# Kernel tuning notes

Measured on AMD Instinct MI355X. Metric: run time of the kernel, lower is better.

The kernel has to match this reference:

```python
import jax, jax.numpy as jnp
import numpy as np

TOP_K = 8
CAPACITY = 512  # >> mean load (T*K/E = 256); overflow probability is negligible

def _silu(x):
    return x * jax.nn.sigmoid(x)

def setup_inputs() -> dict:
    key = jax.random.key(0)
    ks = jax.random.split(key, 7)
    B, S, H, E, I, Is = 2, 1024, 1024, 64, 512, 2048
    s = 0.05
    return {
        "hidden_states": jax.random.normal(ks[0], (B, S, H), jnp.float32),
        "gate_w": jax.random.normal(ks[1], (H, E), jnp.float32) * s,
        "shared_gate_w": jax.random.normal(ks[2], (H, 1), jnp.float32) * s,
        "shared_gate_up_w": jax.random.normal(ks[3], (H, 2 * Is), jnp.float32) * s,
        "shared_down_w": jax.random.normal(ks[4], (Is, H), jnp.float32) * s,
        "expert_gate_up_w": jax.random.normal(ks[5], (E, H, 2 * I), jnp.float32) * s,
        "expert_down_w": jax.random.normal(ks[6], (E, I, H), jnp.float32) * s,
    }

def reference(hidden_states, gate_w, shared_gate_w, shared_gate_up_w, shared_down_w, expert_gate_up_w, expert_down_w):
    B, S, H = hidden_states.shape
    x = hidden_states.reshape(-1, H)                      # [T,H]
    T = x.shape[0]
    E = gate_w.shape[1]
    Is = shared_gate_up_w.shape[1] // 2
    I = expert_gate_up_w.shape[2] // 2

    # ---- shared expert (SwiGLU) with sigmoid token gate ----
    gu = x @ shared_gate_up_w                              # [T,2Is]
    shared = (_silu(gu[:, :Is]) * gu[:, Is:]) @ shared_down_w
    shared = shared * jax.nn.sigmoid(x @ shared_gate_w)    # [T,H]

    # ---- router: fp32 softmax -> top-k -> renormalize ----
    logits = x @ gate_w                                    # [T,E]
    probs = jax.nn.softmax(logits.astype(jnp.float32), axis=-1)
    w, idx = jax.lax.top_k(probs, TOP_K)                   # [T,K]
    w = (w / jnp.sum(w, axis=-1, keepdims=True)).astype(x.dtype)

    # ---- dispatch tokens to per-expert buffers (gather/scatter) ----
    e_flat = idx.reshape(-1)                               # [A] assignments
    w_flat = w.reshape(-1)
    A = e_flat.shape[0]
    tok = jnp.arange(A) // TOP_K                           # source token per assignment
    onehot = jax.nn.one_hot(e_flat, E, dtype=jnp.int32)    # [A,E]
    pos = jnp.take_along_axis(jnp.cumsum(onehot, axis=0) - 1, e_flat[:, None], axis=1)[:, 0]
    slot = jnp.minimum(pos, CAPACITY)                      # overflow -> dummy slot
    buf = jnp.zeros((E, CAPACITY + 1, H), x.dtype).at[e_flat, slot].set(x[tok])

    # ---- grouped expert SwiGLU ----
    gu_e = jnp.einsum('ech,ehf->ecf', buf, expert_gate_up_w)   # [E,C+1,2I]
    act = _silu(gu_e[..., :I]) * gu_e[..., I:]
    out_e = jnp.einsum('eci,eih->ech', act, expert_down_w)     # [E,C+1,H]

    # ---- combine ----
    y = out_e[e_flat, slot] * w_flat[:, None]              # [A,H]
    y = jnp.where((pos < CAPACITY)[:, None], y, jnp.zeros_like(y))
    y = y.reshape(T, TOP_K, H).sum(axis=1)                 # [T,H]

    return (y + shared).reshape(B, S, H)
```

## Files before the change

### kernel.cpp

```cpp
#include <hip/hip_runtime.h>
#include <math.h>

#define T_TOK 2048
#define H_DIM 1024
#define E_NUM 64
#define KTOP 8
#define CAP  512
#define I_DIM 512
#define IS_DIM 2048

#define LDSTR 40

typedef __attribute__((ext_vector_type(8))) _Float16 half8;
typedef __attribute__((ext_vector_type(4))) _Float16 half4v;
typedef __attribute__((ext_vector_type(4))) float f32x4;

__device__ __forceinline__ float sigm(float x){ return 1.f/(1.f+__expf(-x)); }

__global__ __launch_bounds__(256)
void k_tcvt(const float* __restrict__ S, _Float16* __restrict__ D, int K, int N)
{
  __shared__ float T[64][65];
  const size_t so = (size_t)blockIdx.z*K*N;
  const int n0 = blockIdx.x*64, k0 = blockIdx.y*64;
  const int tid = threadIdx.x;
  #pragma unroll
  for (int i=0;i<4;++i){
    int id = tid + i*256;
    int r = id >> 4, c = (id & 15)*4;
    float4 v = *(const float4*)(S + so + (size_t)(k0+r)*N + n0 + c);
    T[r][c]=v.x; T[r][c+1]=v.y; T[r][c+2]=v.z; T[r][c+3]=v.w;
  }
  __syncthreads();
  #pragma unroll
  for (int i=0;i<2;++i){
    int id = tid + i*256;
    int n = id >> 3, kc = (id & 7)*8;
    half8 h;
    #pragma unroll
    for (int j=0;j<8;++j) h[j] = (_Float16)T[kc+j][n];
    *(half8*)(D + so + (size_t)(n0+n)*K + k0 + kc) = h;
  }
}

__global__ __launch_bounds__(256)
void k_cvtx(const float* __restrict__ X, _Float16* __restrict__ Xh)
{
  size_t i = ((size_t)blockIdx.x*256 + threadIdx.x)*4;
  float4 v = *(const float4*)(X + i);
  half4v h = { (_Float16)v.x, (_Float16)v.y, (_Float16)v.z, (_Float16)v.w };
  *(half4v*)(Xh + i) = h;
}

__global__ __launch_bounds__(256)
void k_logits(const float* __restrict__ X, const float* __restrict__ GW,
              const float* __restrict__ SGW, float* __restrict__ logits,
              float* __restrict__ gate_tok)
{
  __shared__ float Xs[32*33];
  __shared__ float Ws[32*64];
  __shared__ float SGWs[32];
  __shared__ float red[256];
  const int tid = threadIdx.x;
  const int t0 = blockIdx.x * 32;
  const int tx = tid & 15, ty = tid >> 4;
  const int tg = tid & 31, qq = tid >> 5;
  float acc[2][4] = {};
  float gacc = 0.f;

  for (int k0 = 0; k0 < H_DIM; k0 += 32) {
    {
      int row = tid >> 3, c4 = (tid & 7)*4;
      float4 v = *(const float4*)(X + (size_t)(t0+row)*H_DIM + k0 + c4);
      Xs[row*33+c4+0]=v.x; Xs[row*33+c4+1]=v.y; Xs[row*33+c4+2]=v.z; Xs[row*33+c4+3]=v.w;
    }
    #pragma unroll
    for (int i=0;i<2;++i){
      int id = tid + i*256;
      int kk = id >> 4, c4 = (id & 15)*4;
      *(float4*)(Ws + kk*64 + c4) = *(const float4*)(GW + (size_t)(k0+kk)*E_NUM + c4);
    }
    if (tid < 32) SGWs[tid] = SGW[k0 + tid];
    __syncthreads();
    #pragma unroll 8
    for (int k=0;k<32;++k){
      float b[4];
      #pragma unroll
      for(int j=0;j<4;++j) b[j] = Ws[k*64 + tx*4 + j];
      #pragma unroll
      for(int i=0;i<2;++i){
        float a = Xs[(ty*2+i)*33 + k];
        #pragma unroll
        for(int j=0;j<4;++j) acc[i][j] = fmaf(a, b[j], acc[i][j]);
      }
    }
    #pragma unroll
    for (int k=0;k<4;++k)
      gacc = fmaf(Xs[tg*33 + qq*4 + k], SGWs[qq*4+k], gacc);
    __syncthreads();
  }
  #pragma unroll
  for(int i=0;i<2;++i){
    float4 o = {acc[i][0],acc[i][1],acc[i][2],acc[i][3]};
    *(float4*)(logits + (size_t)(t0+ty*2+i)*E_NUM + tx*4) = o;
  }
  red[tid] = gacc; __syncthreads();
  if (tid < 32) {
    float g = 0.f;
    #pragma unroll
    for (int p=0;p<8;++p) g += red[tid + p*32];
    gate_tok[t0+tid] = sigm(g);
  }
}

__global__ __launch_bounds__(256)
void k_topk(const float* __restrict__ logits,
            int* __restrict__ counts, int* __restrict__ etok, float* __restrict__ ew)
{
  const int tid = threadIdx.x;
  const int lane = tid & 63, w = tid >> 6;
  const int t = blockIdx.x*4 + w;
  float curv = logits[(size_t)t*E_NUM + lane];
  int curi = lane;
  float topv[KTOP]; int topi[KTOP];
  #pragma unroll
  for (int r = 0; r < KTOP; ++r) {
    float bv = curv; int bi = curi;
    #pragma unroll
    for (int off = 32; off > 0; off >>= 1) {
      float ov = __shfl_xor(bv, off);
      int oi = __shfl_xor(bi, off);
      if (ov > bv || (ov == bv && oi < bi)) { bv = ov; bi = oi; }
    }
    topv[r] = bv; topi[r] = bi;
    if (curi == bi) curv = -INFINITY;
  }
  if (lane == 0) {
    float m = topv[0], s = 0.f, wv[KTOP];
    #pragma unroll
    for (int r = 0; r < KTOP; ++r){ wv[r] = __expf(topv[r]-m); s += wv[r]; }
    float inv = 1.f/s;
    for (int r = 0; r < KTOP; ++r) {
      int ee = topi[r];
      int pos = atomicAdd(&counts[ee], 1);
      if (pos < CAP) {
        etok[ee*CAP + pos] = t;
        ew[ee*CAP + pos] = wv[r]*inv;
      }
    }
  }
}


__device__ __forceinline__ void loadA2(const _Float16* __restrict__ base, int ldk, int k0,
                                       int tid, half8 r[2]) {
  #pragma unroll
  for (int i=0;i<2;++i){
    int id = tid + i*256;
    int m = id >> 2, kc = (id & 3)*8;
    r[i] = *(const half8*)(base + (size_t)m*ldk + k0 + kc);
  }
}
__device__ __forceinline__ void storeA(_Float16* As, int tid, const half8 r[2]) {
  #pragma unroll
  for (int i=0;i<2;++i){
    int id = tid + i*256;
    int m = id >> 2, kc = (id & 3)*8;
    *(half8*)(As + m*LDSTR + kc) = r[i];
  }
}
__device__ __forceinline__ void loadB2(const _Float16* __restrict__ Bt, int ldk,
                                       int r0, int r1, int k0, int tid, half8 r[2]) {
  #pragma unroll
  for (int i=0;i<2;++i){
    int id = tid + i*256;
    int n = id >> 2, kc = (id & 3)*8;
    int grow = (n < 64) ? (r0 + n) : (r1 + n - 64);
    r[i] = *(const half8*)(Bt + (size_t)grow*ldk + k0 + kc);
  }
}
__device__ __forceinline__ void storeB(_Float16* Bs, int tid, const half8 r[2]) {
  #pragma unroll
  for (int i=0;i<2;++i){
    int id = tid + i*256;
    int n = id >> 2, c = id & 3;
    *(half8*)(Bs + n*LDSTR + ((c ^ ((n>>3)&3))*8)) = r[i];
  }
}

__device__ __forceinline__ void mfma_tiles_h(const _Float16* As, const _Float16* Bs,
                                             int wy, const int* bidx, int lane, f32x4 acc[4][4])
{
  const int lm = lane & 15, q = lane >> 4;
  half8 a[4];
  #pragma unroll
  for (int mt = 0; mt < 4; ++mt)
    a[mt] = *(const half8*)(As + (wy*64 + mt*16 + lm)*LDSTR + q*8);
  #pragma unroll
  for (int nt = 0; nt < 4; ++nt) {
    int n = bidx[nt]*16 + lm;
    half8 b = *(const half8*)(Bs + n*LDSTR + ((q ^ ((n>>3)&3))*8));
    #pragma unroll
    for (int mt = 0; mt < 4; ++mt)
      acc[mt][nt] = __builtin_amdgcn_mfma_f32_16x16x32_f16(a[mt], b, acc[mt][nt], 0,0,0);
  }
}

#define DECL_LDS \
  __shared__ __align__(16) _Float16 As[128*LDSTR]; \
  __shared__ __align__(16) _Float16 Bs[128*LDSTR];

#define ZERO_ACC \
  f32x4 acc[4][4]; \
  _Pragma("unroll") for (int a_=0;a_<4;++a_) _Pragma("unroll") for (int b_=0;b_<4;++b_) \
    acc[a_][b_] = (f32x4){0.f,0.f,0.f,0.f};

__global__ __launch_bounds__(256,3)
void k_gu_shared(const _Float16* __restrict__ Xh, const _Float16* __restrict__ Wt,
                 _Float16* __restrict__ O)
{
  DECL_LDS
  const int tid = threadIdx.x, lane = tid & 63, wave = tid >> 6;
  const int wx = wave & 1, wy = wave >> 1;
  const int m0 = blockIdx.y * 128;
  const int gn0 = blockIdx.x * 64;
  ZERO_ACC
  const int bidx[4] = {2*wx, 2*wx+1, 4+2*wx, 5+2*wx};
  const _Float16* Ab = Xh + (size_t)m0*H_DIM;

  half8 ra[2], rb[2];
  loadA2(Ab, H_DIM, 0, tid, ra);
  loadB2(Wt, H_DIM, gn0, IS_DIM + gn0, 0, tid, rb);
  for (int k0 = 0; k0 < H_DIM; k0 += 32) {
    storeA(As, tid, ra); storeB(Bs, tid, rb);
    __syncthreads();
    if (k0 + 32 < H_DIM) {
      loadA2(Ab, H_DIM, k0+32, tid, ra);
      loadB2(Wt, H_DIM, gn0, IS_DIM + gn0, k0+32, tid, rb);
    }
    mfma_tiles_h(As, Bs, wy, bidx, lane, acc);
    __syncthreads();
  }
  const int lm = lane & 15, q = lane >> 4;
  #pragma unroll
  for (int mt = 0; mt < 4; ++mt) {
    int m = m0 + wy*64 + mt*16 + q*4;
    #pragma unroll
    for (int jj = 0; jj < 2; ++jj) {
      int col = gn0 + (2*wx + jj)*16 + lm;
      #pragma unroll
      for (int r = 0; r < 4; ++r) {
        float g = acc[mt][jj][r], u = acc[mt][2+jj][r];
        O[(size_t)(m + r)*IS_DIM + col] = (_Float16)(g * sigm(g) * u);
      }
    }
  }
}

__global__ __launch_bounds__(256,3)
void k_dn_shared(const _Float16* __restrict__ S, const _Float16* __restrict__ Wt,
                 const float* __restrict__ gate_tok, float* __restrict__ OUT)
{
  DECL_LDS
  const int tid = threadIdx.x, lane = tid & 63, wave = tid >> 6;
  const int wx = wave & 1, wy = wave >> 1;
  const int m0 = blockIdx.y * 128;
  const int n0 = blockIdx.x * 128;
  ZERO_ACC
  const int bidx[4] = {4*wx, 4*wx+1, 4*wx+2, 4*wx+3};
  const _Float16* Ab = S + (size_t)m0*IS_DIM;

  half8 ra[2], rb[2];
  loadA2(Ab, IS_DIM, 0, tid, ra);
  loadB2(Wt, IS_DIM, n0, n0 + 64, 0, tid, rb);
  for (int k0 = 0; k0 < IS_DIM; k0 += 32) {
    storeA(As, tid, ra); storeB(Bs, tid, rb);
    __syncthreads();
    if (k0 + 32 < IS_DIM) {
      loadA2(Ab, IS_DIM, k0+32, tid, ra);
      loadB2(Wt, IS_DIM, n0, n0 + 64, k0+32, tid, rb);
    }
    mfma_tiles_h(As, Bs, wy, bidx, lane, acc);
    __syncthreads();
  }
  const int lm = lane & 15, q = lane >> 4;
  #pragma unroll
  for (int mt = 0; mt < 4; ++mt) {
    int m = m0 + wy*64 + mt*16 + q*4;
    #pragma unroll
    for (int r = 0; r < 4; ++r) {
      float gt = gate_tok[m + r];
      #pragma unroll
      for (int nt = 0; nt < 4; ++nt) {
        int col = n0 + wx*64 + nt*16 + lm;
        OUT[(size_t)(m + r)*H_DIM + col] = acc[mt][nt][r] * gt;
      }
    }
  }
}

__global__ __launch_bounds__(256,3)
void k_gu_expert(const _Float16* __restrict__ Xh, const _Float16* __restrict__ Wt,
                 const int* __restrict__ counts, const int* __restrict__ etok,
                 _Float16* __restrict__ O, int e_base)
{
  const int el = blockIdx.z, e = e_base + el;
  int cnt = counts[e]; if (cnt > CAP) cnt = CAP;
  const int m0 = blockIdx.y * 128;
  if (m0 >= cnt) return;
  const int gn0 = blockIdx.x * 64;
  DECL_LDS
  const int tid = threadIdx.x, lane = tid & 63, wave = tid >> 6;
  const int wx = wave & 1, wy = wave >> 1;
  ZERO_ACC
  const int bidx[4] = {2*wx, 2*wx+1, 4+2*wx, 5+2*wx};
  const _Float16* Wb = Wt + (size_t)e*H_DIM*(2*I_DIM);

  int t2[2];
  #pragma unroll
  for (int i = 0; i < 2; ++i) {
    int m = m0 + ((tid + i*256) >> 2);
    t2[i] = (m < cnt) ? etok[e*CAP + m] : -1;
  }

  half8 ra[2], rb[2];
  #pragma unroll
  for (int i=0;i<2;++i){
    int kc = ((tid + i*256) & 3)*8;
    ra[i] = (t2[i] >= 0) ? *(const half8*)(Xh + (size_t)t2[i]*H_DIM + kc)
                         : (half8){0,0,0,0,0,0,0,0};
  }
  loadB2(Wb, H_DIM, gn0, I_DIM + gn0, 0, tid, rb);
  for (int k0 = 0; k0 < H_DIM; k0 += 32) {
    storeA(As, tid, ra); storeB(Bs, tid, rb);
    __syncthreads();
    if (k0 + 32 < H_DIM) {
      #pragma unroll
      for (int i=0;i<2;++i){
        int kc = ((tid + i*256) & 3)*8;
        ra[i] = (t2[i] >= 0) ? *(const half8*)(Xh + (size_t)t2[i]*H_DIM + k0 + 32 + kc)
                             : (half8){0,0,0,0,0,0,0,0};
      }
      loadB2(Wb, H_DIM, gn0, I_DIM + gn0, k0+32, tid, rb);
    }
    mfma_tiles_h(As, Bs, wy, bidx, lane, acc);
    __syncthreads();
  }
  const int lm = lane & 15, q = lane >> 4;
  #pragma unroll
  for (int mt = 0; mt < 4; ++mt) {
    int m = m0 + wy*64 + mt*16 + q*4;
    #pragma unroll
    for (int jj = 0; jj < 2; ++jj) {
      int col = gn0 + (2*wx + jj)*16 + lm;
      #pragma unroll
      for (int r = 0; r < 4; ++r) {
        if (m + r < cnt) {
          float g = acc[mt][jj][r], u = acc[mt][2+jj][r];
          O[((size_t)el*CAP + m + r)*I_DIM + col] = (_Float16)(g * sigm(g) * u);
        }
      }
    }
  }
}

__global__ __launch_bounds__(256,3)
void k_dn_expert(const _Float16* __restrict__ G, const _Float16* __restrict__ Wt,
                 const int* __restrict__ counts, const int* __restrict__ etok,
                 const float* __restrict__ ew, float* __restrict__ OUT, int e_base)
{
  const int el = blockIdx.z, e = e_base + el;
  int cnt = counts[e]; if (cnt > CAP) cnt = CAP;
  const int m0 = blockIdx.y * 128;
  if (m0 >= cnt) return;
  const int n0 = blockIdx.x * 128;
  DECL_LDS
  const int tid = threadIdx.x, lane = tid & 63, wave = tid >> 6;
  const int wx = wave & 1, wy = wave >> 1;
  ZERO_ACC
  const int bidx[4] = {4*wx, 4*wx+1, 4*wx+2, 4*wx+3};
  const _Float16* Wb = Wt + (size_t)e*I_DIM*H_DIM;
  const _Float16* Ab = G + ((size_t)el*CAP + m0)*I_DIM;

  bool ok2[2];
  #pragma unroll
  for (int i=0;i<2;++i) ok2[i] = (m0 + ((tid + i*256) >> 2)) < cnt;

  half8 ra[2], rb[2];
  #pragma unroll
  for (int i=0;i<2;++i){
    int id = tid + i*256;
    int m = id >> 2, kc = (id & 3)*8;
    ra[i] = ok2[i] ? *(const half8*)(Ab + (size_t)m*I_DIM + kc) : (half8){0,0,0,0,0,0,0,0};
  }
  loadB2(Wb, I_DIM, n0, n0 + 64, 0, tid, rb);
  for (int k0 = 0; k0 < I_DIM; k0 += 32) {
    storeA(As, tid, ra); storeB(Bs, tid, rb);
    __syncthreads();
    if (k0 + 32 < I_DIM) {
      #pragma unroll
      for (int i=0;i<2;++i){
        int id = tid + i*256;
        int m = id >> 2, kc = (id & 3)*8;
        ra[i] = ok2[i] ? *(const half8*)(Ab + (size_t)m*I_DIM + k0 + 32 + kc) : (half8){0,0,0,0,0,0,0,0};
      }
      loadB2(Wb, I_DIM, n0, n0 + 64, k0+32, tid, rb);
    }
    mfma_tiles_h(As, Bs, wy, bidx, lane, acc);
    __syncthreads();
  }
  const int lm = lane & 15, q = lane >> 4;
  #pragma unroll
  for (int mt = 0; mt < 4; ++mt) {
    int m = m0 + wy*64 + mt*16 + q*4;
    #pragma unroll
    for (int r = 0; r < 4; ++r) {
      if (m + r < cnt) {
        float w = ew[e*CAP + m + r];
        int tok = etok[e*CAP + m + r];
        float* op = OUT + (size_t)tok*H_DIM;
        #pragma unroll
        for (int nt = 0; nt < 4; ++nt) {
          int col = n0 + wx*64 + nt*16 + lm;
          atomicAdd(op + col, acc[mt][nt][r] * w);
        }
      }
    }
  }
}

extern "C" void kernel_launch(void* const* d_in, const int* in_sizes, int n_in,
                              void* d_out, int out_size, void* d_ws, size_t ws_size,
                              hipStream_t stream) {
  const float* x    = (const float*)d_in[0];
  const float* gw   = (const float*)d_in[1];
  const float* sgw  = (const float*)d_in[2];
  const float* sguw = (const float*)d_in[3];
  const float* sdw  = (const float*)d_in[4];
  const float* eguw = (const float*)d_in[5];
  const float* edw  = (const float*)d_in[6];
  float* out = (float*)d_out;

  char* ws = (char*)d_ws;
  int*   counts   = (int*)(ws + 0);
  int*   etok     = (int*)(ws + 4096);
  float* ew       = (float*)(ws + 4096 + 131072);
  float* gate_tok = (float*)(ws + 4096 + 2*131072);
  float* logits   = (float*)(ws + (512u<<10));
  _Float16* plane  = (_Float16*)(ws + (1u<<20));
  _Float16* Xh     = (_Float16*)(ws + (16u<<20));
  _Float16* sguwT  = (_Float16*)(ws + (24u<<20));
  _Float16* sdwT   = (_Float16*)(ws + (32u<<20));
  _Float16* eguwT  = (_Float16*)(ws + (40u<<20));
  _Float16* edwT   = (_Float16*)(ws + (168u<<20));

  hipMemsetAsync(counts, 0, E_NUM*sizeof(int), stream);
  k_cvtx<<<T_TOK*H_DIM/1024, 256, 0, stream>>>(x, Xh);
  k_tcvt<<<dim3(4096/64, 1024/64, 1),  256, 0, stream>>>(sguw, sguwT, 1024, 4096);
  k_tcvt<<<dim3(1024/64, 2048/64, 1),  256, 0, stream>>>(sdw,  sdwT,  2048, 1024);
  k_tcvt<<<dim3(1024/64, 1024/64, 64), 256, 0, stream>>>(eguw, eguwT, 1024, 1024);
  k_tcvt<<<dim3(1024/64,  512/64, 64), 256, 0, stream>>>(edw,  edwT,   512, 1024);
  k_logits<<<T_TOK/32, 256, 0, stream>>>(x, gw, sgw, logits, gate_tok);
  k_topk<<<T_TOK/4, 256, 0, stream>>>(logits, counts, etok, ew);
  k_gu_shared<<<dim3(IS_DIM/64, T_TOK/128), 256, 0, stream>>>(Xh, sguwT, plane);
  k_dn_shared<<<dim3(H_DIM/128, T_TOK/128), 256, 0, stream>>>(plane, sdwT, gate_tok, out);
  for (int g = 0; g < 4; ++g) {
    k_gu_expert<<<dim3(I_DIM/64, CAP/128, 16), 256, 0, stream>>>(Xh, eguwT, counts, etok, plane, g*16);
    k_dn_expert<<<dim3(H_DIM/128, CAP/128, 16), 256, 0, stream>>>(plane, edwT, counts, etok, ew, out, g*16);
  }
}
```

Baseline: 966.1 us.

## Fuse router, use direct-to-LDS double-buffered GEMMs, replace atomics with combine kernel

Merges the logits and top-k kernels into one router kernel that also records per-assignment slots and weights. All GEMMs now stage tiles with global_load_lds into double-buffered LDS with BK=64 and XOR swizzling, replacing the register-staged single buffer. The per-group expert launches become a single launch over all 64 experts. The expert down projection now writes per-slot outputs to a buffer and a separate combine kernel sums them per token, replacing float atomics. This trades more LDS per block (lower occupancy) and an extra fp32 intermediate buffer for fewer launches, less atomic contention and better load overlap.

```diff
diff --git a/kernel.cpp b/kernel.cpp
--- a/kernel.cpp
+++ b/kernel.cpp
@@ -8,14 +8,19 @@
 #define CAP  512
 #define I_DIM 512
 #define IS_DIM 2048
-
-#define LDSTR 40
+#define BK 64
 
 typedef __attribute__((ext_vector_type(8))) _Float16 half8;
 typedef __attribute__((ext_vector_type(4))) _Float16 half4v;
 typedef __attribute__((ext_vector_type(4))) float f32x4;
 
 __device__ __forceinline__ float sigm(float x){ return 1.f/(1.f+__expf(-x)); }
+
+__device__ __forceinline__ void gl16(const _Float16* g, _Float16* l) {
+  __builtin_amdgcn_global_load_lds((const __attribute__((address_space(1))) void*)g,
+                                   (__attribute__((address_space(3))) void*)l,
+                                   16, 0, 0);
+}
 
 __global__ __launch_bounds__(256)
 void k_tcvt(const float* __restrict__ S, _Float16* __restrict__ D, int K, int N)
@@ -53,79 +58,47 @@
 }
 
 __global__ __launch_bounds__(256)
-void k_logits(const float* __restrict__ X, const float* __restrict__ GW,
-              const float* __restrict__ SGW, float* __restrict__ logits,
-              float* __restrict__ gate_tok)
-{
-  __shared__ float Xs[32*33];
-  __shared__ float Ws[32*64];
-  __shared__ float SGWs[32];
-  __shared__ float red[256];
-  const int tid = threadIdx.x;
-  const int t0 = blockIdx.x * 32;
-  const int tx = tid & 15, ty = tid >> 4;
-  const int tg = tid & 31, qq = tid >> 5;
-  float acc[2][4] = {};
-  float gacc = 0.f;
-
-  for (int k0 = 0; k0 < H_DIM; k0 += 32) {
-    {
-      int row = tid >> 3, c4 = (tid & 7)*4;
-      float4 v = *(const float4*)(X + (size_t)(t0+row)*H_DIM + k0 + c4);
-      Xs[row*33+c4+0]=v.x; Xs[row*33+c4+1]=v.y; Xs[row*33+c4+2]=v.z; Xs[row*33+c4+3]=v.w;
-    }
-    #pragma unroll
-    for (int i=0;i<2;++i){
-      int id = tid + i*256;
-      int kk = id >> 4, c4 = (id & 15)*4;
-      *(float4*)(Ws + kk*64 + c4) = *(const float4*)(GW + (size_t)(k0+kk)*E_NUM + c4);
-    }
-    if (tid < 32) SGWs[tid] = SGW[k0 + tid];
-    __syncthreads();
-    #pragma unroll 8
-    for (int k=0;k<32;++k){
-      float b[4];
-      #pragma unroll
-      for(int j=0;j<4;++j) b[j] = Ws[k*64 + tx*4 + j];
-      #pragma unroll
-      for(int i=0;i<2;++i){
-        float a = Xs[(ty*2+i)*33 + k];
-        #pragma unroll
-        for(int j=0;j<4;++j) acc[i][j] = fmaf(a, b[j], acc[i][j]);
-      }
-    }
-    #pragma unroll
-    for (int k=0;k<4;++k)
-      gacc = fmaf(Xs[tg*33 + qq*4 + k], SGWs[qq*4+k], gacc);
-    __syncthreads();
-  }
-  #pragma unroll
-  for(int i=0;i<2;++i){
-    float4 o = {acc[i][0],acc[i][1],acc[i][2],acc[i][3]};
-    *(float4*)(logits + (size_t)(t0+ty*2+i)*E_NUM + tx*4) = o;
-  }
-  red[tid] = gacc; __syncthreads();
-  if (tid < 32) {
-    float g = 0.f;
-    #pragma unroll
-    for (int p=0;p<8;++p) g += red[tid + p*32];
-    gate_tok[t0+tid] = sigm(g);
-  }
-}
-
-__global__ __launch_bounds__(256)
-void k_topk(const float* __restrict__ logits,
-            int* __restrict__ counts, int* __restrict__ etok, float* __restrict__ ew)
-{
-  const int tid = threadIdx.x;
-  const int lane = tid & 63, w = tid >> 6;
-  const int t = blockIdx.x*4 + w;
-  float curv = logits[(size_t)t*E_NUM + lane];
-  int curi = lane;
+void k_router(const float* __restrict__ X, const float* __restrict__ GW,
+              const float* __restrict__ SGW, int* __restrict__ counts,
+              int* __restrict__ etok, float* __restrict__ gate_tok,
+              int* __restrict__ asg, float* __restrict__ aw)
+{
+  __shared__ float Xs[4][1024];
+  __shared__ float part[4][4][64];
+  const int tid = threadIdx.x, w = tid>>6, lane = tid&63;
+  const int t0 = blockIdx.x*4;
+  #pragma unroll
+  for (int i=0;i<4;++i){
+    int idx = tid + i*256;
+    *(float4*)(&Xs[0][0] + idx*4) = *(const float4*)(X + (size_t)t0*H_DIM + idx*4);
+  }
+  __syncthreads();
+  {
+    float a0=0.f,a1=0.f,a2=0.f,a3=0.f;
+    const int kb = w*256;
+    #pragma unroll 4
+    for (int k=0;k<256;++k){
+      float gv = GW[(size_t)(kb+k)*E_NUM + lane];
+      a0 = fmaf(Xs[0][kb+k], gv, a0);
+      a1 = fmaf(Xs[1][kb+k], gv, a1);
+      a2 = fmaf(Xs[2][kb+k], gv, a2);
+      a3 = fmaf(Xs[3][kb+k], gv, a3);
+    }
+    part[w][0][lane]=a0; part[w][1][lane]=a1; part[w][2][lane]=a2; part[w][3][lane]=a3;
+  }
+  float g = 0.f;
+  #pragma unroll
+  for (int i=0;i<16;++i) g = fmaf(Xs[w][lane+64*i], SGW[lane+64*i], g);
+  #pragma unroll
+  for (int off=32;off;off>>=1) g += __shfl_xor(g, off);
+  __syncthreads();
+  const int t = t0 + w;
+  if (lane==0) gate_tok[t] = sigm(g);
+  float curv = part[0][w][lane]+part[1][w][lane]+part[2][w][lane]+part[3][w][lane];
   float topv[KTOP]; int topi[KTOP];
   #pragma unroll
   for (int r = 0; r < KTOP; ++r) {
-    float bv = curv; int bi = curi;
+    float bv = curv; int bi = lane;
     #pragma unroll
     for (int off = 32; off > 0; off >>= 1) {
       float ov = __shfl_xor(bv, off);
@@ -133,7 +106,7 @@
       if (ov > bv || (ov == bv && oi < bi)) { bv = ov; bi = oi; }
     }
     topv[r] = bv; topi[r] = bi;
-    if (curi == bi) curv = -INFINITY;
+    if (lane == bi) curv = -INFINITY;
   }
   if (lane == 0) {
     float m = topv[0], s = 0.f, wv[KTOP];
@@ -143,103 +116,107 @@
     for (int r = 0; r < KTOP; ++r) {
       int ee = topi[r];
       int pos = atomicAdd(&counts[ee], 1);
-      if (pos < CAP) {
-        etok[ee*CAP + pos] = t;
-        ew[ee*CAP + pos] = wv[r]*inv;
-      }
-    }
-  }
-}
-
-
-__device__ __forceinline__ void loadA2(const _Float16* __restrict__ base, int ldk, int k0,
-                                       int tid, half8 r[2]) {
-  #pragma unroll
-  for (int i=0;i<2;++i){
-    int id = tid + i*256;
-    int m = id >> 2, kc = (id & 3)*8;
-    r[i] = *(const half8*)(base + (size_t)m*ldk + k0 + kc);
-  }
-}
-__device__ __forceinline__ void storeA(_Float16* As, int tid, const half8 r[2]) {
-  #pragma unroll
-  for (int i=0;i<2;++i){
-    int id = tid + i*256;
-    int m = id >> 2, kc = (id & 3)*8;
-    *(half8*)(As + m*LDSTR + kc) = r[i];
-  }
-}
-__device__ __forceinline__ void loadB2(const _Float16* __restrict__ Bt, int ldk,
-                                       int r0, int r1, int k0, int tid, half8 r[2]) {
-  #pragma unroll
-  for (int i=0;i<2;++i){
-    int id = tid + i*256;
-    int n = id >> 2, kc = (id & 3)*8;
-    int grow = (n < 64) ? (r0 + n) : (r1 + n - 64);
-    r[i] = *(const half8*)(Bt + (size_t)grow*ldk + k0 + kc);
-  }
-}
-__device__ __forceinline__ void storeB(_Float16* Bs, int tid, const half8 r[2]) {
-  #pragma unroll
-  for (int i=0;i<2;++i){
-    int id = tid + i*256;
-    int n = id >> 2, c = id & 3;
-    *(half8*)(Bs + n*LDSTR + ((c ^ ((n>>3)&3))*8)) = r[i];
-  }
-}
-
-__device__ __forceinline__ void mfma_tiles_h(const _Float16* As, const _Float16* Bs,
-                                             int wy, const int* bidx, int lane, f32x4 acc[4][4])
-{
-  const int lm = lane & 15, q = lane >> 4;
-  half8 a[4];
-  #pragma unroll
-  for (int mt = 0; mt < 4; ++mt)
-    a[mt] = *(const half8*)(As + (wy*64 + mt*16 + lm)*LDSTR + q*8);
-  #pragma unroll
-  for (int nt = 0; nt < 4; ++nt) {
-    int n = bidx[nt]*16 + lm;
-    half8 b = *(const half8*)(Bs + n*LDSTR + ((q ^ ((n>>3)&3))*8));
-    #pragma unroll
-    for (int mt = 0; mt < 4; ++mt)
-      acc[mt][nt] = __builtin_amdgcn_mfma_f32_16x16x32_f16(a[mt], b, acc[mt][nt], 0,0,0);
-  }
-}
-
-#define DECL_LDS \
-  __shared__ __align__(16) _Float16 As[128*LDSTR]; \
-  __shared__ __align__(16) _Float16 Bs[128*LDSTR];
-
-#define ZERO_ACC \
-  f32x4 acc[4][4]; \
-  _Pragma("unroll") for (int a_=0;a_<4;++a_) _Pragma("unroll") for (int b_=0;b_<4;++b_) \
-    acc[a_][b_] = (f32x4){0.f,0.f,0.f,0.f};
-
-__global__ __launch_bounds__(256,3)
+      bool ok = (pos < CAP);
+      if (ok) etok[ee*CAP + pos] = t;
+      asg[t*KTOP + r] = ok ? (ee*CAP + pos) : -1;
+      aw[t*KTOP + r]  = wv[r]*inv;
+    }
+  }
+}
+
+
+template<int MT>
+__device__ __forceinline__ void stageA_lin(const _Float16* __restrict__ Ab, int ldk, int k0,
+                                           int tid, _Float16* Asb)
+{
+  const int w = tid>>6, l = tid&63, sub = l>>3, gc = (l&7) ^ sub;
+  #pragma unroll
+  for (int j=0;j<MT;++j){
+    int r = (w*MT + j)*8 + sub;
+    gl16(Ab + (size_t)r*ldk + k0 + gc*8, Asb + (w*MT+j)*512 + l*8);
+  }
+}
+__device__ __forceinline__ void stageA_ptr(const _Float16* const* bj, int k0,
+                                           int tid, _Float16* Asb)
+{
+  const int w = tid>>6, l = tid&63, gc = (l&7) ^ (l>>3);
+  #pragma unroll
+  for (int j=0;j<4;++j)
+    gl16(bj[j] + k0 + gc*8, Asb + (w*4+j)*512 + l*8);
+}
+__device__ __forceinline__ void stageB(const _Float16* __restrict__ Bt, int ldk,
+                                       int r0, int r1, int k0, int tid, _Float16* Bsb)
+{
+  const int w = tid>>6, l = tid&63, sub = l>>3, gc = (l&7) ^ sub;
+  #pragma unroll
+  for (int j=0;j<4;++j){
+    int r = (w*4+j)*8 + sub;
+    int grow = (r < 64) ? (r0 + r) : (r1 + r - 64);
+    gl16(Bt + (size_t)grow*ldk + k0 + gc*8, Bsb + (w*4+j)*512 + l*8);
+  }
+}
+
+template<int MT>
+__device__ __forceinline__ void mfma_bk64(const _Float16* As, const _Float16* Bs,
+                                          int wy, const int* bidx, int lane,
+                                          f32x4 acc[][4])
+{
+  const int lm = lane & 15, q = lane >> 4, h = lm & 7;
+  half8 a[2][MT], b[2][4];
+  #pragma unroll
+  for (int kk=0;kk<2;++kk){
+    #pragma unroll
+    for (int mt=0;mt<MT;++mt){
+      int r = wy*(MT*16) + mt*16 + lm;
+      int ch = ((kk<<2)|q) ^ h;
+      a[kk][mt] = *(const half8*)(As + r*BK + ch*8);
+    }
+    #pragma unroll
+    for (int nt=0;nt<4;++nt){
+      int n = bidx[nt]*16 + lm;
+      int ch = ((kk<<2)|q) ^ h;
+      b[kk][nt] = *(const half8*)(Bs + n*BK + ch*8);
+    }
+  }
+  #pragma unroll
+  for (int kk=0;kk<2;++kk)
+    #pragma unroll
+    for (int nt=0;nt<4;++nt)
+      #pragma unroll
+      for (int mt=0;mt<MT;++mt)
+        acc[mt][nt] = __builtin_amdgcn_mfma_f32_16x16x32_f16(a[kk][mt], b[kk][nt], acc[mt][nt], 0,0,0);
+}
+
+#define ZACC(MT_) \
+  f32x4 acc[MT_][4]; \
+  _Pragma("unroll") for (int a_=0;a_<MT_;++a_) \
+  _Pragma("unroll") for (int b_=0;b_<4;++b_) acc[a_][b_] = (f32x4){0.f,0.f,0.f,0.f};
+
+__global__ __launch_bounds__(256,2)
 void k_gu_shared(const _Float16* __restrict__ Xh, const _Float16* __restrict__ Wt,
                  _Float16* __restrict__ O)
 {
-  DECL_LDS
+  __shared__ __align__(16) _Float16 As[2][128*BK];
+  __shared__ __align__(16) _Float16 Bs[2][128*BK];
   const int tid = threadIdx.x, lane = tid & 63, wave = tid >> 6;
   const int wx = wave & 1, wy = wave >> 1;
-  const int m0 = blockIdx.y * 128;
-  const int gn0 = blockIdx.x * 64;
-  ZERO_ACC
+  const int m0 = blockIdx.y * 128, gn0 = blockIdx.x * 64;
+  ZACC(4)
   const int bidx[4] = {2*wx, 2*wx+1, 4+2*wx, 5+2*wx};
   const _Float16* Ab = Xh + (size_t)m0*H_DIM;
 
-  half8 ra[2], rb[2];
-  loadA2(Ab, H_DIM, 0, tid, ra);
-  loadB2(Wt, H_DIM, gn0, IS_DIM + gn0, 0, tid, rb);
-  for (int k0 = 0; k0 < H_DIM; k0 += 32) {
-    storeA(As, tid, ra); storeB(Bs, tid, rb);
+  stageA_lin<4>(Ab, H_DIM, 0, tid, As[0]);
+  stageB(Wt, H_DIM, gn0, IS_DIM+gn0, 0, tid, Bs[0]);
+  __syncthreads();
+  int cur = 0;
+  for (int k0 = 0; k0 < H_DIM; k0 += BK) {
+    if (k0 + BK < H_DIM) {
+      stageA_lin<4>(Ab, H_DIM, k0+BK, tid, As[cur^1]);
+      stageB(Wt, H_DIM, gn0, IS_DIM+gn0, k0+BK, tid, Bs[cur^1]);
+    }
+    mfma_bk64<4>(As[cur], Bs[cur], wy, bidx, lane, acc);
     __syncthreads();
-    if (k0 + 32 < H_DIM) {
-      loadA2(Ab, H_DIM, k0+32, tid, ra);
-      loadB2(Wt, H_DIM, gn0, IS_DIM + gn0, k0+32, tid, rb);
-    }
-    mfma_tiles_h(As, Bs, wy, bidx, lane, acc);
-    __syncthreads();
+    cur ^= 1;
   }
   const int lm = lane & 15, q = lane >> 4;
   #pragma unroll
@@ -261,32 +238,32 @@
 void k_dn_shared(const _Float16* __restrict__ S, const _Float16* __restrict__ Wt,
                  const float* __restrict__ gate_tok, float* __restrict__ OUT)
 {
-  DECL_LDS
+  __shared__ __align__(16) _Float16 As[2][64*BK];
+  __shared__ __align__(16) _Float16 Bs[2][128*BK];
   const int tid = threadIdx.x, lane = tid & 63, wave = tid >> 6;
   const int wx = wave & 1, wy = wave >> 1;
-  const int m0 = blockIdx.y * 128;
-  const int n0 = blockIdx.x * 128;
-  ZERO_ACC
+  const int m0 = blockIdx.y * 64, n0 = blockIdx.x * 128;
+  ZACC(2)
   const int bidx[4] = {4*wx, 4*wx+1, 4*wx+2, 4*wx+3};
   const _Float16* Ab = S + (size_t)m0*IS_DIM;
 
-  half8 ra[2], rb[2];
-  loadA2(Ab, IS_DIM, 0, tid, ra);
-  loadB2(Wt, IS_DIM, n0, n0 + 64, 0, tid, rb);
-  for (int k0 = 0; k0 < IS_DIM; k0 += 32) {
-    storeA(As, tid, ra); storeB(Bs, tid, rb);
+  stageA_lin<2>(Ab, IS_DIM, 0, tid, As[0]);
+  stageB(Wt, IS_DIM, n0, n0+64, 0, tid, Bs[0]);
+  __syncthreads();
+  int cur = 0;
+  for (int k0 = 0; k0 < IS_DIM; k0 += BK) {
+    if (k0 + BK < IS_DIM) {
+      stageA_lin<2>(Ab, IS_DIM, k0+BK, tid, As[cur^1]);
+      stageB(Wt, IS_DIM, n0, n0+64, k0+BK, tid, Bs[cur^1]);
+    }
+    mfma_bk64<2>(As[cur], Bs[cur], wy, bidx, lane, acc);
     __syncthreads();
-    if (k0 + 32 < IS_DIM) {
-      loadA2(Ab, IS_DIM, k0+32, tid, ra);
-      loadB2(Wt, IS_DIM, n0, n0 + 64, k0+32, tid, rb);
-    }
-    mfma_tiles_h(As, Bs, wy, bidx, lane, acc);
-    __syncthreads();
+    cur ^= 1;
   }
   const int lm = lane & 15, q = lane >> 4;
   #pragma unroll
-  for (int mt = 0; mt < 4; ++mt) {
-    int m = m0 + wy*64 + mt*16 + q*4;
+  for (int mt = 0; mt < 2; ++mt) {
+    int m = m0 + wy*32 + mt*16 + q*4;
     #pragma unroll
     for (int r = 0; r < 4; ++r) {
       float gt = gate_tok[m + r];
@@ -299,52 +276,46 @@
   }
 }
 
-__global__ __launch_bounds__(256,3)
+__global__ __launch_bounds__(256,2)
 void k_gu_expert(const _Float16* __restrict__ Xh, const _Float16* __restrict__ Wt,
                  const int* __restrict__ counts, const int* __restrict__ etok,
-                 _Float16* __restrict__ O, int e_base)
-{
-  const int el = blockIdx.z, e = e_base + el;
+                 const _Float16* __restrict__ zp, _Float16* __restrict__ O)
+{
+  const int e = blockIdx.z;
   int cnt = counts[e]; if (cnt > CAP) cnt = CAP;
   const int m0 = blockIdx.y * 128;
   if (m0 >= cnt) return;
-  const int gn0 = blockIdx.x * 64;
-  DECL_LDS
+  __shared__ __align__(16) _Float16 As[2][128*BK];
+  __shared__ __align__(16) _Float16 Bs[2][128*BK];
   const int tid = threadIdx.x, lane = tid & 63, wave = tid >> 6;
   const int wx = wave & 1, wy = wave >> 1;
-  ZERO_ACC
+  const int gn0 = blockIdx.x * 64;
+  ZACC(4)
   const int bidx[4] = {2*wx, 2*wx+1, 4+2*wx, 5+2*wx};
   const _Float16* Wb = Wt + (size_t)e*H_DIM*(2*I_DIM);
 
-  int t2[2];
-  #pragma unroll
-  for (int i = 0; i < 2; ++i) {
-    int m = m0 + ((tid + i*256) >> 2);
-    t2[i] = (m < cnt) ? etok[e*CAP + m] : -1;
-  }
-
-  half8 ra[2], rb[2];
-  #pragma unroll
-  for (int i=0;i<2;++i){
-    int kc = ((tid + i*256) & 3)*8;
-    ra[i] = (t2[i] >= 0) ? *(const half8*)(Xh + (size_t)t2[i]*H_DIM + kc)
-                         : (half8){0,0,0,0,0,0,0,0};
-  }
-  loadB2(Wb, H_DIM, gn0, I_DIM + gn0, 0, tid, rb);
-  for (int k0 = 0; k0 < H_DIM; k0 += 32) {
-    storeA(As, tid, ra); storeB(Bs, tid, rb);
+  const _Float16* bj[4];
+  {
+    const int w = tid>>6, l = tid&63, sub = l>>3;
+    #pragma unroll
+    for (int j=0;j<4;++j){
+      int m = m0 + (w*4+j)*8 + sub;
+      int t = (m < cnt) ? etok[e*CAP + m] : -1;
+      bj[j] = (t >= 0) ? (Xh + (size_t)t*H_DIM) : zp;
+    }
+  }
+  stageA_ptr(bj, 0, tid, As[0]);
+  stageB(Wb, H_DIM, gn0, I_DIM+gn0, 0, tid, Bs[0]);
+  __syncthreads();
+  int cur = 0;
+  for (int k0 = 0; k0 < H_DIM; k0 += BK) {
+    if (k0 + BK < H_DIM) {
+      stageA_ptr(bj, k0+BK, tid, As[cur^1]);
+      stageB(Wb, H_DIM, gn0, I_DIM+gn0, k0+BK, tid, Bs[cur^1]);
+    }
+    mfma_bk64<4>(As[cur], Bs[cur], wy, bidx, lane, acc);
     __syncthreads();
-    if (k0 + 32 < H_DIM) {
-      #pragma unroll
-      for (int i=0;i<2;++i){
-        int kc = ((tid + i*256) & 3)*8;
-        ra[i] = (t2[i] >= 0) ? *(const half8*)(Xh + (size_t)t2[i]*H_DIM + k0 + 32 + kc)
-                             : (half8){0,0,0,0,0,0,0,0};
-      }
-      loadB2(Wb, H_DIM, gn0, I_DIM + gn0, k0+32, tid, rb);
-    }
-    mfma_tiles_h(As, Bs, wy, bidx, lane, acc);
-    __syncthreads();
+    cur ^= 1;
   }
   const int lm = lane & 15, q = lane >> 4;
   #pragma unroll
@@ -357,57 +328,52 @@
       for (int r = 0; r < 4; ++r) {
         if (m + r < cnt) {
           float g = acc[mt][jj][r], u = acc[mt][2+jj][r];
-          O[((size_t)el*CAP + m + r)*I_DIM + col] = (_Float16)(g * sigm(g) * u);
+          O[((size_t)e*CAP + m + r)*I_DIM + col] = (_Float16)(g * sigm(g) * u);
         }
       }
     }
   }
 }
 
-__global__ __launch_bounds__(256,3)
+__global__ __launch_bounds__(256,2)
 void k_dn_expert(const _Float16* __restrict__ G, const _Float16* __restrict__ Wt,
-                 const int* __restrict__ counts, const int* __restrict__ etok,
-                 const float* __restrict__ ew, float* __restrict__ OUT, int e_base)
-{
-  const int el = blockIdx.z, e = e_base + el;
+                 const int* __restrict__ counts, const _Float16* __restrict__ zp,
+                 float* __restrict__ Oe)
+{
+  const int e = blockIdx.z;
   int cnt = counts[e]; if (cnt > CAP) cnt = CAP;
   const int m0 = blockIdx.y * 128;
   if (m0 >= cnt) return;
   const int n0 = blockIdx.x * 128;
-  DECL_LDS
+  __shared__ __align__(16) _Float16 As[2][128*BK];
+  __shared__ __align__(16) _Float16 Bs[2][128*BK];
   const int tid = threadIdx.x, lane = tid & 63, wave = tid >> 6;
   const int wx = wave & 1, wy = wave >> 1;
-  ZERO_ACC
+  ZACC(4)
   const int bidx[4] = {4*wx, 4*wx+1, 4*wx+2, 4*wx+3};
   const _Float16* Wb = Wt + (size_t)e*I_DIM*H_DIM;
-  const _Float16* Ab = G + ((size_t)el*CAP + m0)*I_DIM;
-
-  bool ok2[2];
-  #pragma unroll
-  for (int i=0;i<2;++i) ok2[i] = (m0 + ((tid + i*256) >> 2)) < cnt;
-
-  half8 ra[2], rb[2];
-  #pragma unroll
-  for (int i=0;i<2;++i){
-    int id = tid + i*256;
-    int m = id >> 2, kc = (id & 3)*8;
-    ra[i] = ok2[i] ? *(const half8*)(Ab + (size_t)m*I_DIM + kc) : (half8){0,0,0,0,0,0,0,0};
-  }
-  loadB2(Wb, I_DIM, n0, n0 + 64, 0, tid, rb);
-  for (int k0 = 0; k0 < I_DIM; k0 += 32) {
-    storeA(As, tid, ra); storeB(Bs, tid, rb);
+
+  const _Float16* bj[4];
+  {
+    const int w = tid>>6, l = tid&63, sub = l>>3;
+    #pragma unroll
+    for (int j=0;j<4;++j){
+      int m = m0 + (w*4+j)*8 + sub;
+      bj[j] = (m < cnt) ? (G + (size_t)(e*CAP + m)*I_DIM) : zp;
+    }
+  }
+  stageA_ptr(bj, 0, tid, As[0]);
+  stageB(Wb, I_DIM, n0, n0+64, 0, tid, Bs[0]);
+  __syncthreads();
+  int cur = 0;
+  for (int k0 = 0; k0 < I_DIM; k0 += BK) {
+    if (k0 + BK < I_DIM) {
+      stageA_ptr(bj, k0+BK, tid, As[cur^1]);
+      stageB(Wb, I_DIM, n0, n0+64, k0+BK, tid, Bs[cur^1]);
+    }
+    mfma_bk64<4>(As[cur], Bs[cur], wy, bidx, lane, acc);
     __syncthreads();
-    if (k0 + 32 < I_DIM) {
-      #pragma unroll
-      for (int i=0;i<2;++i){
-        int id = tid + i*256;
-        int m = id >> 2, kc = (id & 3)*8;
-        ra[i] = ok2[i] ? *(const half8*)(Ab + (size_t)m*I_DIM + k0 + 32 + kc) : (half8){0,0,0,0,0,0,0,0};
-      }
-      loadB2(Wb, I_DIM, n0, n0 + 64, k0+32, tid, rb);
-    }
-    mfma_tiles_h(As, Bs, wy, bidx, lane, acc);
-    __syncthreads();
+    cur ^= 1;
   }
   const int lm = lane & 15, q = lane >> 4;
   #pragma unroll
@@ -416,17 +382,36 @@
     #pragma unroll
     for (int r = 0; r < 4; ++r) {
       if (m + r < cnt) {
-        float w = ew[e*CAP + m + r];
-        int tok = etok[e*CAP + m + r];
-        float* op = OUT + (size_t)tok*H_DIM;
         #pragma unroll
         for (int nt = 0; nt < 4; ++nt) {
           int col = n0 + wx*64 + nt*16 + lm;
-          atomicAdd(op + col, acc[mt][nt][r] * w);
+          Oe[(size_t)(e*CAP + m + r)*H_DIM + col] = acc[mt][nt][r];
         }
       }
     }
   }
+}
+
+__global__ __launch_bounds__(256)
+void k_combine(const float* __restrict__ Oe, const int* __restrict__ asg,
+               const float* __restrict__ aw, float* __restrict__ OUT)
+{
+  __shared__ int sa[KTOP]; __shared__ float sw[KTOP];
+  const int t = blockIdx.x, tid = threadIdx.x;
+  if (tid < KTOP){ sa[tid] = asg[t*KTOP + tid]; sw[tid] = aw[t*KTOP + tid]; }
+  __syncthreads();
+  float4 acc = *(const float4*)(OUT + (size_t)t*H_DIM + tid*4);
+  #pragma unroll
+  for (int r = 0; r < KTOP; ++r) {
+    int a = sa[r];
+    if (a >= 0) {
+      float wv = sw[r];
+      float4 v = *(const float4*)(Oe + (size_t)a*H_DIM + tid*4);
+      acc.x = fmaf(v.x, wv, acc.x); acc.y = fmaf(v.y, wv, acc.y);
+      acc.z = fmaf(v.z, wv, acc.z); acc.w = fmaf(v.w, wv, acc.w);
+    }
+  }
+  *(float4*)(OUT + (size_t)t*H_DIM + tid*4) = acc;
 }
 
 extern "C" void kernel_launch(void* const* d_in, const int* in_sizes, int n_in,
@@ -442,30 +427,31 @@
   float* out = (float*)d_out;
 
   char* ws = (char*)d_ws;
-  int*   counts   = (int*)(ws + 0);
-  int*   etok     = (int*)(ws + 4096);
-  float* ew       = (float*)(ws + 4096 + 131072);
-  float* gate_tok = (float*)(ws + 4096 + 2*131072);
-  float* logits   = (float*)(ws + (512u<<10));
-  _Float16* plane  = (_Float16*)(ws + (1u<<20));
-  _Float16* Xh     = (_Float16*)(ws + (16u<<20));
-  _Float16* sguwT  = (_Float16*)(ws + (24u<<20));
-  _Float16* sdwT   = (_Float16*)(ws + (32u<<20));
-  _Float16* eguwT  = (_Float16*)(ws + (40u<<20));
-  _Float16* edwT   = (_Float16*)(ws + (168u<<20));
-
-  hipMemsetAsync(counts, 0, E_NUM*sizeof(int), stream);
+  int*      counts   = (int*)(ws + 0);
+  _Float16* zp       = (_Float16*)(ws + 4096);
+  int*      etok     = (int*)(ws + 32768);
+  int*      asg      = (int*)(ws + 163840);
+  float*    aw       = (float*)(ws + 229376);
+  float*    gate_tok = (float*)(ws + 294912);
+  _Float16* Xh       = (_Float16*)(ws + (1u<<20));
+  _Float16* plane    = (_Float16*)(ws + (8u<<20));
+  _Float16* actg     = (_Float16*)(ws + (16u<<20));
+  float*    Oe       = (float*)(ws + (48u<<20));
+  _Float16* sguwT    = (_Float16*)(ws + (176u<<20));
+  _Float16* sdwT     = (_Float16*)(ws + (184u<<20));
+  _Float16* eguwT    = (_Float16*)(ws + (192u<<20));
+  _Float16* edwT     = (_Float16*)(ws + (320u<<20));
+
+  hipMemsetAsync(ws, 0, 32768, stream);
   k_cvtx<<<T_TOK*H_DIM/1024, 256, 0, stream>>>(x, Xh);
+  k_router<<<T_TOK/4, 256, 0, stream>>>(x, gw, sgw, counts, etok, gate_tok, asg, aw);
   k_tcvt<<<dim3(4096/64, 1024/64, 1),  256, 0, stream>>>(sguw, sguwT, 1024, 4096);
   k_tcvt<<<dim3(1024/64, 2048/64, 1),  256, 0, stream>>>(sdw,  sdwT,  2048, 1024);
   k_tcvt<<<dim3(1024/64, 1024/64, 64), 256, 0, stream>>>(eguw, eguwT, 1024, 1024);
   k_tcvt<<<dim3(1024/64,  512/64, 64), 256, 0, stream>>>(edw,  edwT,   512, 1024);
-  k_logits<<<T_TOK/32, 256, 0, stream>>>(x, gw, sgw, logits, gate_tok);
-  k_topk<<<T_TOK/4, 256, 0, stream>>>(logits, counts, etok, ew);
   k_gu_shared<<<dim3(IS_DIM/64, T_TOK/128), 256, 0, stream>>>(Xh, sguwT, plane);
-  k_dn_shared<<<dim3(H_DIM/128, T_TOK/128), 256, 0, stream>>>(plane, sdwT, gate_tok, out);
-  for (int g = 0; g < 4; ++g) {
-    k_gu_expert<<<dim3(I_DIM/64, CAP/128, 16), 256, 0, stream>>>(Xh, eguwT, counts, etok, plane, g*16);
-    k_dn_expert<<<dim3(H_DIM/128, CAP/128, 16), 256, 0, stream>>>(plane, edwT, counts, etok, ew, out, g*16);
-  }
-}
+  k_dn_shared<<<dim3(H_DIM/128, T_TOK/64), 256, 0, stream>>>(plane, sdwT, gate_tok, out);
+  k_gu_expert<<<dim3(I_DIM/64, CAP/128, E_NUM), 256, 0, stream>>>(Xh, eguwT, counts, etok, zp, actg);
+  k_dn_expert<<<dim3(H_DIM/128, CAP/128, E_NUM), 256, 0, stream>>>(actg, edwT, counts, zp, Oe);
+  k_combine<<<T_TOK, 256, 0, stream>>>(Oe, asg, aw, out);
+}
```

Measured after the change: 850.3 us. 1.14x faster.
